# Optimization experiments

Measured on AMD Instinct MI355X. Metric: run time of the kernel, lower is better.

## Reference

```python
import jax, jax.numpy as jnp
import numpy as np

B, T, L = 4096, 512, 16


def setup_inputs() -> dict:
    key = jax.random.key(0)
    k1, k2, k3, k4 = jax.random.split(key, 4)
    x = jax.random.normal(k1, (B, T, L), dtype=jnp.float32)
    trans = jax.random.uniform(k2, (L, L), dtype=jnp.float32)
    label = jax.random.randint(k3, (B, T), 0, L, dtype=jnp.int32)
    length = jax.random.randint(k4, (B,), 1, T + 1, dtype=jnp.int32)
    return {"x": x, "trans": trans, "label": label, "length": length}


def _crf_loss(x, trans, label, length):
    b, t, l = x.shape
    # valid-position mask [B, T]
    mask = (jnp.arange(t)[None, :] < length[:, None]).astype(x.dtype)
    x = x * mask[:, :, None]  # mask emissions like the original

    # ---- gold path score ----
    # emission (point) score: sum_t x[b, t, label[b, t]] over valid t
    emit = jnp.take_along_axis(x, label[:, :, None].astype(jnp.int32), axis=2)[..., 0]
    point_score = jnp.sum(emit * mask, axis=1, keepdims=True)  # [B, 1]
    # transition score: sum over consecutive valid label pairs
    pair_mask = mask[:, 1:]  # both t and t+1 valid iff t+1 valid (monotone mask)
    trans_pairs = trans[label[:, :-1], label[:, 1:]]  # [B, T-1]
    trans_score = jnp.sum(trans_pairs * pair_mask, axis=1, keepdims=True)  # [B, 1]
    label_score = point_score + trans_score  # [B, 1]

    # ---- partition function via forward algorithm (scan over time) ----
    alpha0 = x[:, 0, :]  # [B, L]
    xs = jnp.swapaxes(x[:, 1:, :], 0, 1)  # [T-1, B, L]

    def step(alpha, x_t):
        # logsumexp over previous label axis of alpha[b, i] + trans[i, j]
        new = jax.nn.logsumexp(alpha[:, :, None] + trans[None, :, :], axis=1) + x_t
        return new, new

    _, ys = jax.lax.scan(step, alpha0, xs)  # ys: [T-1, B, L]
    alphas = jnp.concatenate([alpha0[None], ys], axis=0)  # [T, B, L]
    # pick alpha at t = length - 1 for each batch element
    final = alphas[length - 1, jnp.arange(b), :]  # [B, L]
    z = jax.nn.logsumexp(final, axis=1, keepdims=True)  # [B, 1]
    return z - label_score


def reference(x, trans, label, length):
    return _crf_loss(x, trans, label, length)
```

## Files before the change

### kernel.cpp

```cpp
#include <hip/hip_runtime.h>
#include <cstdint>


static constexpr float L2E = 1.4426950408889634f;
static constexpr float LN2 = 0.69314718055994531f;

__device__ __forceinline__ void gload_lds16(const void* g, void* l) {
  __builtin_amdgcn_global_load_lds((const __attribute__((address_space(1))) unsigned int*)g,
                                   (__attribute__((address_space(3))) unsigned int*)l, 16, 0, 0);
}
__device__ __forceinline__ void gload_lds4(const void* g, void* l) {
  __builtin_amdgcn_global_load_lds((const __attribute__((address_space(1))) unsigned int*)g,
                                   (__attribute__((address_space(3))) unsigned int*)l, 4, 0, 0);
}
__device__ __forceinline__ void wait_vm0() { asm volatile("s_waitcnt vmcnt(0)" ::: "memory"); }
__device__ __forceinline__ void wait_vm5() { asm volatile("s_waitcnt vmcnt(5)" ::: "memory"); }

template <int CTRL>
__device__ __forceinline__ float qadd(float v) {
  int x = __builtin_amdgcn_mov_dpp(__builtin_bit_cast(int, v), CTRL, 0xF, 0xF, true);
  return v + __builtin_bit_cast(float, x);
}
__device__ __forceinline__ float rfl(float v) {
  return __builtin_bit_cast(float, __builtin_amdgcn_readfirstlane(__builtin_bit_cast(int, v)));
}

__global__ __launch_bounds__(256, 4) void crf_fwd(
    const float* __restrict__ x, const float* __restrict__ trans,
    const int* __restrict__ label, const int* __restrict__ length,
    float* __restrict__ out) {
  __shared__ float ldsx[4][2][64 * 16];
  __shared__ int   ldsl[4][2][64];
  __shared__ float ldst[256];

  const int tid  = threadIdx.x;
  const int wv   = tid >> 6;
  const int lane = tid & 63;
  const int j    = lane >> 2;
  const int g    = lane & 3;

  ldst[tid] = trans[tid];
  __syncthreads();

  const int b   = blockIdx.x * 4 + wv;
  const int len = length[b];
  const int nch = ((len - 1) >> 6) + 1;

  const float m0 = __builtin_amdgcn_exp2f(trans[(4 * g + 0) * 16 + j] * L2E);
  const float m1 = __builtin_amdgcn_exp2f(trans[(4 * g + 1) * 16 + j] * L2E);
  const float m2 = __builtin_amdgcn_exp2f(trans[(4 * g + 2) * 16 + j] * L2E);
  const float m3 = __builtin_amdgcn_exp2f(trans[(4 * g + 3) * 16 + j] * L2E);

  const int a0 = (16 * g + 0) * 4;
  const int a1 = (16 * g + 4) * 4;
  const int a2 = (16 * g + 8) * 4;
  const int a3 = (16 * g + 12) * 4;

  const char* xb = (const char*)x + (size_t)b * 32768;
  const char* lb = (const char*)label + (size_t)b * 2048;

  auto stage = [&](int c, int buf) {
    const char* gx = xb + c * 4096;
    float* lxp = &ldsx[wv][buf][0];
    gload_lds16(gx + 0 * 1024 + lane * 16, lxp + 0 * 256);
    gload_lds16(gx + 1 * 1024 + lane * 16, lxp + 1 * 256);
    gload_lds16(gx + 2 * 1024 + lane * 16, lxp + 2 * 256);
    gload_lds16(gx + 3 * 1024 + lane * 16, lxp + 3 * 256);
    gload_lds4(lb + c * 256 + lane * 4, &ldsl[wv][buf][0]);
  };

  stage(0, 0);

  float av = 1.0f;
  float R2 = 0.0f;
  float em = 0.0f;
  float ts = 0.0f;
  int lastl = 0;

  for (int c = 0; c < nch; ++c) {
    const int buf = c & 1;
    const bool pre = (c + 1 < nch);
    if (pre) stage(c + 1, buf ^ 1);
    if (pre) wait_vm5(); else wait_vm0();

    float* lx = &ldsx[wv][buf][0];
    int*   ll = &ldsl[wv][buf][0];

    {
      const int gt   = c * 64 + lane;
      const int lblt = ll[lane];
      const int lprv = (lane == 0) ? lastl : ll[lane - 1];
      const float emv = lx[lane * 16 + lblt];
      const float tsv = ldst[lprv * 16 + lblt];
      if (gt < len) em += emv;
      if (gt >= 1 && gt < len) ts += tsv;
      lastl = __shfl(lblt, 63, 64);
    }

    {
      float4* p = (float4*)(lx + lane * 16);
#pragma unroll
      for (int k = 0; k < 4; ++k) {
        float4 v = p[k];
        v.x = __builtin_amdgcn_exp2f(v.x * L2E);
        v.y = __builtin_amdgcn_exp2f(v.y * L2E);
        v.z = __builtin_amdgcn_exp2f(v.z * L2E);
        v.w = __builtin_amdgcn_exp2f(v.w * L2E);
        p[k] = v;
      }
    }

    if (c == 0) av = lx[j];

    const int start = (c == 0) ? 1 : c * 64;
    const int end   = (len - 1 < c * 64 + 63) ? (len - 1) : (c * 64 + 63);
    const int n     = end - start + 1;
    if (n > 0) {
      const float* exp_ = lx + (start & 63) * 16 + j;

      auto step = [&]() {
        const int ai = __builtin_bit_cast(int, av);
        const float g0 = __builtin_bit_cast(float, __builtin_amdgcn_ds_bpermute(a0, ai));
        const float g1 = __builtin_bit_cast(float, __builtin_amdgcn_ds_bpermute(a1, ai));
        const float g2 = __builtin_bit_cast(float, __builtin_amdgcn_ds_bpermute(a2, ai));
        const float g3 = __builtin_bit_cast(float, __builtin_amdgcn_ds_bpermute(a3, ai));
        float v01 = __builtin_fmaf(g1, m1, g0 * m0);
        float v23 = __builtin_fmaf(g3, m3, g2 * m2);
        float v = v01 + v23;
        v = qadd<0xB1>(v);
        v = qadd<0x4E>(v);
        av = v * (*exp_);
        exp_ += 16;
      };

      const int n4 = n >> 2, rem = n & 3;
      for (int q = 0; q < n4; ++q) {
        step(); step(); step(); step();
        const float Cs = rfl(av);
        const float rs = __builtin_amdgcn_rcpf(Cs);
        av *= rs;
        R2 += __builtin_amdgcn_logf(Cs);
      }
      for (int e = 0; e < rem; ++e) step();
    }
  }

  float stot = av;
  stot += __shfl_xor(stot, 1, 64);
  stot += __shfl_xor(stot, 2, 64);
  stot += __shfl_xor(stot, 4, 64);
  stot += __shfl_xor(stot, 8, 64);
  stot += __shfl_xor(stot, 16, 64);
  stot += __shfl_xor(stot, 32, 64);

  em += __shfl_xor(em, 1, 64);
  em += __shfl_xor(em, 2, 64);
  em += __shfl_xor(em, 4, 64);
  em += __shfl_xor(em, 8, 64);
  em += __shfl_xor(em, 16, 64);
  em += __shfl_xor(em, 32, 64);

  ts += __shfl_xor(ts, 1, 64);
  ts += __shfl_xor(ts, 2, 64);
  ts += __shfl_xor(ts, 4, 64);
  ts += __shfl_xor(ts, 8, 64);
  ts += __shfl_xor(ts, 16, 64);
  ts += __shfl_xor(ts, 32, 64);

  const float z2 = R2 + __builtin_amdgcn_logf(stot) - 2.0f;
  const float res = z2 * LN2 - em - ts;
  if (lane == 0) out[b] = res;
}

extern "C" void kernel_launch(void* const* d_in, const int* in_sizes, int n_in,
                              void* d_out, int out_size, void* d_ws, size_t ws_size,
                              hipStream_t stream) {
  const float* x      = (const float*)d_in[0];
  const float* trans  = (const float*)d_in[1];
  const int*   label  = (const int*)d_in[2];
  const int*   length = (const int*)d_in[3];
  float* out = (float*)d_out;
  const int B = in_sizes[3];
  crf_fwd<<<dim3(B / 4), dim3(256), 0, stream>>>(x, trans, label, length, out);
}
```

Before: 251.5 us.

## Replicate alpha across 16-lane rows and use DPP row rotates instead of bpermute

Changes the forward-recursion mapping so each 16-lane row holds the full alpha vector: lane l16 owns label l16 and computes a 16-term dot product with the transition column, gathering neighbours through DPP row_ror moves. This removes the four LDS ds_bpermute round trips and the two-stage quad reduction per time step, replacing them with register-level DPP ops and a longer FMA chain. Renormalisation now also runs after a tail of fewer than four steps, and the final reduction sums within a row, which drops the -2 correction that the old four-fold replication needed. It costs more VALU work per step and 16 transition constants held in registers.

```diff
diff --git a/kernel.cpp b/kernel.cpp
--- a/kernel.cpp
+++ b/kernel.cpp
@@ -17,9 +17,13 @@
 __device__ __forceinline__ void wait_vm5() { asm volatile("s_waitcnt vmcnt(5)" ::: "memory"); }
 
 template <int CTRL>
-__device__ __forceinline__ float qadd(float v) {
-  int x = __builtin_amdgcn_mov_dpp(__builtin_bit_cast(int, v), CTRL, 0xF, 0xF, true);
-  return v + __builtin_bit_cast(float, x);
+__device__ __forceinline__ float dppf(float v) {
+  return __builtin_bit_cast(float,
+      __builtin_amdgcn_mov_dpp(__builtin_bit_cast(int, v), CTRL, 0xF, 0xF, true));
+}
+template <int CTRL>
+__device__ __forceinline__ int dppi(int v) {
+  return __builtin_amdgcn_mov_dpp(v, CTRL, 0xF, 0xF, true);
 }
 __device__ __forceinline__ float rfl(float v) {
   return __builtin_bit_cast(float, __builtin_amdgcn_readfirstlane(__builtin_bit_cast(int, v)));
@@ -36,8 +40,7 @@
   const int tid  = threadIdx.x;
   const int wv   = tid >> 6;
   const int lane = tid & 63;
-  const int j    = lane >> 2;
-  const int g    = lane & 3;
+  const int l16  = lane & 15;
 
   ldst[tid] = trans[tid];
   __syncthreads();
@@ -46,15 +49,37 @@
   const int len = length[b];
   const int nch = ((len - 1) >> 6) + 1;
 
-  const float m0 = __builtin_amdgcn_exp2f(trans[(4 * g + 0) * 16 + j] * L2E);
-  const float m1 = __builtin_amdgcn_exp2f(trans[(4 * g + 1) * 16 + j] * L2E);
-  const float m2 = __builtin_amdgcn_exp2f(trans[(4 * g + 2) * 16 + j] * L2E);
-  const float m3 = __builtin_amdgcn_exp2f(trans[(4 * g + 3) * 16 + j] * L2E);
-
-  const int a0 = (16 * g + 0) * 4;
-  const int a1 = (16 * g + 4) * 4;
-  const int a2 = (16 * g + 8) * 4;
-  const int a3 = (16 * g + 12) * 4;
+  const int i1  = dppi<0x121>(l16);
+  const int i2  = dppi<0x122>(l16);
+  const int i3  = dppi<0x123>(l16);
+  const int i4  = dppi<0x124>(l16);
+  const int i5  = dppi<0x125>(l16);
+  const int i6  = dppi<0x126>(l16);
+  const int i7  = dppi<0x127>(l16);
+  const int i8  = dppi<0x128>(l16);
+  const int i9  = dppi<0x129>(l16);
+  const int i10 = dppi<0x12A>(l16);
+  const int i11 = dppi<0x12B>(l16);
+  const int i12 = dppi<0x12C>(l16);
+  const int i13 = dppi<0x12D>(l16);
+  const int i14 = dppi<0x12E>(l16);
+  const int i15 = dppi<0x12F>(l16);
+  const float m0  = __builtin_amdgcn_exp2f(trans[l16 * 16 + l16] * L2E);
+  const float m1  = __builtin_amdgcn_exp2f(trans[i1  * 16 + l16] * L2E);
+  const float m2  = __builtin_amdgcn_exp2f(trans[i2  * 16 + l16] * L2E);
+  const float m3  = __builtin_amdgcn_exp2f(trans[i3  * 16 + l16] * L2E);
+  const float m4  = __builtin_amdgcn_exp2f(trans[i4  * 16 + l16] * L2E);
+  const float m5  = __builtin_amdgcn_exp2f(trans[i5  * 16 + l16] * L2E);
+  const float m6  = __builtin_amdgcn_exp2f(trans[i6  * 16 + l16] * L2E);
+  const float m7  = __builtin_amdgcn_exp2f(trans[i7  * 16 + l16] * L2E);
+  const float m8  = __builtin_amdgcn_exp2f(trans[i8  * 16 + l16] * L2E);
+  const float m9  = __builtin_amdgcn_exp2f(trans[i9  * 16 + l16] * L2E);
+  const float m10 = __builtin_amdgcn_exp2f(trans[i10 * 16 + l16] * L2E);
+  const float m11 = __builtin_amdgcn_exp2f(trans[i11 * 16 + l16] * L2E);
+  const float m12 = __builtin_amdgcn_exp2f(trans[i12 * 16 + l16] * L2E);
+  const float m13 = __builtin_amdgcn_exp2f(trans[i13 * 16 + l16] * L2E);
+  const float m14 = __builtin_amdgcn_exp2f(trans[i14 * 16 + l16] * L2E);
+  const float m15 = __builtin_amdgcn_exp2f(trans[i15 * 16 + l16] * L2E);
 
   const char* xb = (const char*)x + (size_t)b * 32768;
   const char* lb = (const char*)label + (size_t)b * 2048;
@@ -76,6 +101,31 @@
   float em = 0.0f;
   float ts = 0.0f;
   int lastl = 0;
+
+  auto step = [&](float xe) {
+    float a0 = av * m0;
+    float a1 = dppf<0x124>(av) * m4;
+    float a2 = dppf<0x128>(av) * m8;
+    float a3 = dppf<0x12C>(av) * m12;
+    a0 = __builtin_fmaf(dppf<0x121>(av), m1,  a0);
+    a1 = __builtin_fmaf(dppf<0x125>(av), m5,  a1);
+    a2 = __builtin_fmaf(dppf<0x129>(av), m9,  a2);
+    a3 = __builtin_fmaf(dppf<0x12D>(av), m13, a3);
+    a0 = __builtin_fmaf(dppf<0x122>(av), m2,  a0);
+    a1 = __builtin_fmaf(dppf<0x126>(av), m6,  a1);
+    a2 = __builtin_fmaf(dppf<0x12A>(av), m10, a2);
+    a3 = __builtin_fmaf(dppf<0x12E>(av), m14, a3);
+    a0 = __builtin_fmaf(dppf<0x123>(av), m3,  a0);
+    a1 = __builtin_fmaf(dppf<0x127>(av), m7,  a1);
+    a2 = __builtin_fmaf(dppf<0x12B>(av), m11, a2);
+    a3 = __builtin_fmaf(dppf<0x12F>(av), m15, a3);
+    av = ((a0 + a1) + (a2 + a3)) * xe;
+  };
+  auto renorm = [&]() {
+    const float C = rfl(av);
+    av *= __builtin_amdgcn_rcpf(C);
+    R2 += __builtin_amdgcn_logf(C);
+  };
 
   for (int c = 0; c < nch; ++c) {
     const int buf = c & 1;
@@ -110,48 +160,34 @@
       }
     }
 
-    if (c == 0) av = lx[j];
+    if (c == 0) av = lx[l16];
 
     const int start = (c == 0) ? 1 : c * 64;
     const int end   = (len - 1 < c * 64 + 63) ? (len - 1) : (c * 64 + 63);
-    const int n     = end - start + 1;
+    int n = end - start + 1;
     if (n > 0) {
-      const float* exp_ = lx + (start & 63) * 16 + j;
-
-      auto step = [&]() {
-        const int ai = __builtin_bit_cast(int, av);
-        const float g0 = __builtin_bit_cast(float, __builtin_amdgcn_ds_bpermute(a0, ai));
-        const float g1 = __builtin_bit_cast(float, __builtin_amdgcn_ds_bpermute(a1, ai));
-        const float g2 = __builtin_bit_cast(float, __builtin_amdgcn_ds_bpermute(a2, ai));
-        const float g3 = __builtin_bit_cast(float, __builtin_amdgcn_ds_bpermute(a3, ai));
-        float v01 = __builtin_fmaf(g1, m1, g0 * m0);
-        float v23 = __builtin_fmaf(g3, m3, g2 * m2);
-        float v = v01 + v23;
-        v = qadd<0xB1>(v);
-        v = qadd<0x4E>(v);
-        av = v * (*exp_);
-        exp_ += 16;
-      };
-
-      const int n4 = n >> 2, rem = n & 3;
-      for (int q = 0; q < n4; ++q) {
-        step(); step(); step(); step();
-        const float Cs = rfl(av);
-        const float rs = __builtin_amdgcn_rcpf(Cs);
-        av *= rs;
-        R2 += __builtin_amdgcn_logf(Cs);
+      const float* xp = lx + (start & 63) * 16 + l16;
+      while (n >= 4) {
+        step(xp[0]);
+        step(xp[16]);
+        step(xp[32]);
+        step(xp[48]);
+        xp += 64;
+        n -= 4;
+        renorm();
       }
-      for (int e = 0; e < rem; ++e) step();
+      if (n > 0) {
+        for (int e = 0; e < n; ++e) step(xp[e * 16]);
+        renorm();
+      }
     }
   }
 
   float stot = av;
-  stot += __shfl_xor(stot, 1, 64);
-  stot += __shfl_xor(stot, 2, 64);
-  stot += __shfl_xor(stot, 4, 64);
-  stot += __shfl_xor(stot, 8, 64);
-  stot += __shfl_xor(stot, 16, 64);
-  stot += __shfl_xor(stot, 32, 64);
+  stot += dppf<0x128>(stot);
+  stot += dppf<0x124>(stot);
+  stot += dppf<0x122>(stot);
+  stot += dppf<0x121>(stot);
 
   em += __shfl_xor(em, 1, 64);
   em += __shfl_xor(em, 2, 64);
@@ -167,7 +203,7 @@
   ts += __shfl_xor(ts, 16, 64);
   ts += __shfl_xor(ts, 32, 64);
 
-  const float z2 = R2 + __builtin_amdgcn_logf(stot) - 2.0f;
+  const float z2 = R2 + __builtin_amdgcn_logf(stot);
   const float res = z2 * LN2 - em - ts;
   if (lane == 0) out[b] = res;
 }
```

Result: slower. 269.5 us (+7.2%).
